# Optimization experiments

Measured on AMD Instinct MI355X. Metric: run time of the kernel, lower is better.

The kernel has to match this reference:

```python
import jax, jax.numpy as jnp
import numpy as np

DIM = 768
NUM_HEADS = 12
HEAD_DIM = DIM // NUM_HEADS
EPS = 1e-5


def setup_inputs() -> dict:
    key = jax.random.key(0)
    ks = jax.random.split(key, 9)
    s = 1.0 / np.sqrt(DIM)
    x = jax.random.normal(ks[0], (8, 1024, DIM), dtype=jnp.float32)
    Wq = jax.random.uniform(ks[1], (DIM, DIM), jnp.float32, -s, s)
    bq = jax.random.uniform(ks[2], (DIM,), jnp.float32, -s, s)
    Wk = jax.random.uniform(ks[3], (DIM, DIM), jnp.float32, -s, s)
    bk = jax.random.uniform(ks[4], (DIM,), jnp.float32, -s, s)
    Wv = jax.random.uniform(ks[5], (DIM, DIM), jnp.float32, -s, s)
    bv = jax.random.uniform(ks[6], (DIM,), jnp.float32, -s, s)
    Wo = jax.random.uniform(ks[7], (DIM, DIM), jnp.float32, -s, s)
    bo = jax.random.uniform(ks[8], (DIM,), jnp.float32, -s, s)
    ln_g = jnp.ones((DIM,), jnp.float32)
    ln_b = jnp.zeros((DIM,), jnp.float32)
    return {"x": x, "Wq": Wq, "bq": bq, "Wk": Wk, "bk": bk, "Wv": Wv,
            "bv": bv, "Wo": Wo, "bo": bo, "ln_g": ln_g, "ln_b": ln_b}


def _layernorm(h, g, b):
    mu = jnp.mean(h, axis=-1, keepdims=True)
    var = jnp.mean(jnp.square(h - mu), axis=-1, keepdims=True)
    return (h - mu) * jax.lax.rsqrt(var + EPS) * g + b


def reference(x, Wq, bq, Wk, bk, Wv, bv, Wo, bo, ln_g, ln_b):
    B, N, C = x.shape
    H, D = NUM_HEADS, HEAD_DIM
    scaling = D ** -0.5
    q = (x @ Wq.T + bq) * scaling          # [B,N,C]
    k = x @ Wk.T + bk
    v = x @ Wv.T + bv
    q = q.reshape(B, N, H, D).transpose(0, 2, 1, 3)  # [B,H,N,D]
    k = k.reshape(B, N, H, D).transpose(0, 2, 1, 3)
    v = v.reshape(B, N, H, D).transpose(0, 2, 1, 3)
    scores = jnp.einsum('bhnd,bhmd->bhnm', q, k)     # [B,H,N,N]
    probs = jax.nn.softmax(scores.astype(jnp.float32), axis=-1).astype(scores.dtype)
    attn = jnp.einsum('bhnm,bhmd->bhnd', probs, v)   # [B,H,N,D]
    attn = attn.transpose(0, 2, 1, 3).reshape(B, N, C)
    attn = _layernorm(attn, ln_g, ln_b)
    return attn @ Wo.T + bo
```

## Files before the change

### kernel.cpp

```cpp
#include <hip/hip_runtime.h>
#include <hip/hip_bf16.h>
#include <stdint.h>


using short8  = __attribute__((ext_vector_type(8))) short;
using short4v = __attribute__((ext_vector_type(4))) short;
using floatx4 = __attribute__((ext_vector_type(4))) float;

#define LOG2E 1.44269504088896340736f

typedef __attribute__((address_space(3))) uint32_t lds_u32;
typedef const __attribute__((address_space(1))) uint32_t glb_u32;
__device__ __forceinline__ void async_copy16(const void* g, void* l) {
  __builtin_amdgcn_global_load_lds((glb_u32*)g, (lds_u32*)l, 16, 0, 0);
}

__device__ __forceinline__ float b2f(int s) {
  return __builtin_bit_cast(float, (uint32_t)((uint16_t)s) << 16);
}
__device__ __forceinline__ short f2b(float f) {
  uint32_t u = __builtin_bit_cast(uint32_t, f);
  u += 0x7fffu + ((u >> 16) & 1u);
  return (short)(u >> 16);
}
__device__ __forceinline__ uint32_t pk2(float a, float b) {
#if defined(__has_builtin) && __has_builtin(__builtin_amdgcn_cvt_pk_bf16_f32)
  typedef __bf16 bf16x2 __attribute__((ext_vector_type(2)));
  return __builtin_bit_cast(uint32_t, __builtin_amdgcn_cvt_pk_bf16_f32(a, b));
#else
  return (uint32_t)(uint16_t)f2b(a) | ((uint32_t)(uint16_t)f2b(b) << 16);
#endif
}
__device__ __forceinline__ float loadf(const void* p, int idx, bool f32) {
  return f32 ? ((const float*)p)[idx] : b2f(((const short*)p)[idx]);
}
__device__ __forceinline__ short8 load8f(const void* p, int idx) {
  const float* q = (const float*)p + idx;
  float4 x0 = *(const float4*)q, x1 = *(const float4*)(q + 4);
  short8 v = {f2b(x0.x), f2b(x0.y), f2b(x0.z), f2b(x0.w),
              f2b(x1.x), f2b(x1.y), f2b(x1.z), f2b(x1.w)};
  return v;
}

__global__ __launch_bounds__(256) void cvt1_k(
    const void* __restrict__ x, const void* __restrict__ wq,
    const void* __restrict__ wk, const void* __restrict__ wv,
    const void* __restrict__ bq, const void* __restrict__ bk,
    const void* __restrict__ bv, short* __restrict__ xb,
    short* __restrict__ wqkvb, short* __restrict__ bqkvb,
    const unsigned short* __restrict__ probe) {
  if (probe[0] == 0x3F80u) return;
  int idx = blockIdx.x * 256 + threadIdx.x;
  if (idx < 786432) { *(short8*)&xb[idx * 8] = load8f(x, idx * 8); return; }
  idx -= 786432;
  if (idx < 73728) { *(short8*)&wqkvb[idx * 8] = load8f(wq, idx * 8); return; }
  idx -= 73728;
  if (idx < 73728) { *(short8*)&wqkvb[589824 + idx * 8] = load8f(wk, idx * 8); return; }
  idx -= 73728;
  if (idx < 73728) { *(short8*)&wqkvb[1179648 + idx * 8] = load8f(wv, idx * 8); return; }
  idx -= 73728;
  if (idx < 96) { *(short8*)&bqkvb[idx * 8] = load8f(bq, idx * 8); return; }
  idx -= 96;
  if (idx < 96) { *(short8*)&bqkvb[768 + idx * 8] = load8f(bk, idx * 8); return; }
  idx -= 96;
  if (idx < 96) { *(short8*)&bqkvb[1536 + idx * 8] = load8f(bv, idx * 8); return; }
}

__device__ __forceinline__ void gemm_core(const short* __restrict__ Ab,
                                          const short* __restrict__ Bb,
                                          short (*sA)[4096], short (*sB)[4096],
                                          floatx4 (&acc)[4][4]) {
  const int t = threadIdx.x;
  const int w = t >> 6, l = t & 63;
  const int lrow = l & 15, quad = l >> 4;
  const int rw = (w >> 1) * 64, cw = (w & 1) * 64;
  const int ci0 = t, ci1 = 256 + t;
  const int row0 = ci0 >> 2, ch0 = ci0 & 3;
  const int row1 = ci1 >> 2, ch1 = ci1 & 3;

  async_copy16(Ab + row0 * 768 + ch0 * 8, (char*)sA[0] + ci0 * 16);
  async_copy16(Bb + row0 * 768 + ch0 * 8, (char*)sB[0] + ci0 * 16);
  async_copy16(Ab + row1 * 768 + ch1 * 8, (char*)sA[0] + ci1 * 16);
  async_copy16(Bb + row1 * 768 + ch1 * 8, (char*)sB[0] + ci1 * 16);
  __syncthreads();

  for (int it = 0; it < 24; it++) {
    const int cur = it & 1;
    if (it < 23) {
      const int k0 = (it + 1) * 32, nxt = cur ^ 1;
      async_copy16(Ab + row0 * 768 + k0 + ch0 * 8, (char*)sA[nxt] + ci0 * 16);
      async_copy16(Bb + row0 * 768 + k0 + ch0 * 8, (char*)sB[nxt] + ci0 * 16);
      async_copy16(Ab + row1 * 768 + k0 + ch1 * 8, (char*)sA[nxt] + ci1 * 16);
      async_copy16(Bb + row1 * 768 + k0 + ch1 * 8, (char*)sB[nxt] + ci1 * 16);
    }
    short8 af[4], bf[4];
#pragma unroll
    for (int i = 0; i < 4; i++)
      af[i] = *(const short8*)&sA[cur][(rw + i * 16 + lrow) * 32 + quad * 8];
#pragma unroll
    for (int j = 0; j < 4; j++)
      bf[j] = *(const short8*)&sB[cur][(cw + j * 16 + lrow) * 32 + quad * 8];
#pragma unroll
    for (int i = 0; i < 4; i++)
#pragma unroll
      for (int j = 0; j < 4; j++)
        acc[i][j] =
            __builtin_amdgcn_mfma_f32_16x16x32_bf16(af[i], bf[j], acc[i][j], 0, 0, 0);
    __syncthreads();
  }
}

__global__ __launch_bounds__(256, 4) void gemm_qkv_k(
    const void* __restrict__ x, const short* __restrict__ xb,
    const void* __restrict__ Wq, const void* __restrict__ Wk,
    const void* __restrict__ Wv, const short* __restrict__ wqkvb,
    const void* __restrict__ bq, const void* __restrict__ bk,
    const void* __restrict__ bv, const short* __restrict__ bqkvb,
    short* __restrict__ qo, short* __restrict__ ko, short* __restrict__ vo,
    const unsigned short* __restrict__ probe) {
  __shared__ __align__(16) short sA[2][4096];
  __shared__ __align__(16) short sB[2][4096];
  const bool f32 = (probe[0] != 0x3F80u);
  const int atile = blockIdx.x, btile = blockIdx.y;
  const int sel = btile / 6;

  const short* Ab = (f32 ? xb : (const short*)x) + atile * 98304;
  const short* Bb;
  const short* biasb;
  if (f32) {
    Bb = wqkvb + btile * 98304;
    biasb = bqkvb + sel * 768;
  } else {
    const void* Wsel = sel == 0 ? Wq : (sel == 1 ? Wk : Wv);
    Bb = (const short*)Wsel + (btile - sel * 6) * 98304;
    biasb = (const short*)(sel == 0 ? bq : (sel == 1 ? bk : bv));
  }

  floatx4 acc[4][4] = {};
  gemm_core(Ab, Bb, sA, sB, acc);

  const int t = threadIdx.x, w = t >> 6, l = t & 63;
  const int lrow = l & 15, quad = l >> 4;
  const int rw = (w >> 1) * 64, cw = (w & 1) * 64;
  const int nbase = (btile - sel * 6) * 128;
#pragma unroll
  for (int i = 0; i < 4; i++) {
    const int ra0 = atile * 128 + rw + i * 16 + quad * 4;
    const int bidx = ra0 >> 10, n_in_b = ra0 & 1023;
#pragma unroll
    for (int j = 0; j < 4; j++) {
      const int cb = nbase + cw + j * 16 + lrow;
      const float bias = b2f(biasb[cb]);
      const int hh = cb >> 6, dd = cb & 63;
      if (sel == 2) {
        short4v pv;
#pragma unroll
        for (int r = 0; r < 4; r++) pv[r] = f2b(acc[i][j][r] + bias);
        const int n64 = n_in_b & 63;
        const int pos = ((n64 >> 2) & 3) * 8 + (n64 & 32) + ((n64 >> 4) & 1) * 4;
        *(short4v*)&vo[(bidx * 12 + hh) * 65536 + dd * 1024 + (n_in_b & ~63) + pos] = pv;
      } else {
        const int base = (bidx * 12 + hh) * 65536 + dd;
        short* dst = sel == 0 ? qo : ko;
#pragma unroll
        for (int r = 0; r < 4; r++) {
          float v = acc[i][j][r] + bias;
          if (sel == 0) v *= (0.125f * LOG2E);
          dst[base + (n_in_b + r) * 64] = f2b(v);
        }
      }
    }
  }
}

__global__ __launch_bounds__(256, 4) void gemm_out_k(
    const short* __restrict__ ln, const void* __restrict__ Wo,
    const short* __restrict__ wob, const void* __restrict__ bo,
    const short* __restrict__ bob, void* __restrict__ out,
    const unsigned short* __restrict__ probe) {
  __shared__ __align__(16) short sA[2][4096];
  __shared__ __align__(16) short sB[2][4096];
  const bool f32 = (probe[0] != 0x3F80u);
  const int atile = blockIdx.x, btile = blockIdx.y;
  const short* Ab = ln + atile * 98304;
  const short* Bb = (f32 ? wob : (const short*)Wo) + btile * 98304;
  const short* biasb = f32 ? bob : (const short*)bo;

  floatx4 acc[4][4] = {};
  gemm_core(Ab, Bb, sA, sB, acc);

  const int t = threadIdx.x, w = t >> 6, l = t & 63;
  const int lrow = l & 15, quad = l >> 4;
  const int rw = (w >> 1) * 64, cw = (w & 1) * 64;
#pragma unroll
  for (int i = 0; i < 4; i++) {
    const int ra0 = atile * 128 + rw + i * 16 + quad * 4;
#pragma unroll
    for (int j = 0; j < 4; j++) {
      const int cb = btile * 128 + cw + j * 16 + lrow;
      const float bias = b2f(biasb[cb]);
#pragma unroll
      for (int r = 0; r < 4; r++) {
        float v = acc[i][j][r] + bias;
        if (f32) ((float*)out)[(ra0 + r) * 768 + cb] = v;
        else     ((short*)out)[(ra0 + r) * 768 + cb] = f2b(v);
      }
    }
  }
}

__global__ __launch_bounds__(256, 5) void attn_k(const short* __restrict__ q,
                                                 const short* __restrict__ k,
                                                 const short* __restrict__ vt,
                                                 short* __restrict__ o) {
  __shared__ __align__(16) short sMem[2][8192];

  const int t = threadIdx.x, w = t >> 6, l = t & 63;
  const int lrow = l & 15, quad = l >> 4;
  const int bh = blockIdx.x, qt = blockIdx.y;
  const int b = bh / 12, h = bh % 12;
  const short* qb = q + bh * 65536 + qt * 4096;
  const short* kb = k + bh * 65536;
  const short* vb = vt + bh * 65536;

  const int srow = t >> 3, sgc = (t & 7) ^ (srow & 7);
  const short* kst = kb + srow * 64 + sgc * 8;
  const short* vst = vb + srow * 1024 + sgc * 8;

  const int swz0 = (quad ^ (lrow & 7)) * 16;
  const int swz1 = ((4 + quad) ^ (lrow & 7)) * 16;
  const char* s0 = (const char*)&sMem[0][0];
  const char* kp0 = s0 + lrow * 128 + swz0;
  const char* kp1 = s0 + lrow * 128 + swz1;
  const char* vp0 = s0 + 8192 + lrow * 128 + swz0;
  const char* vp1 = s0 + 8192 + lrow * 128 + swz1;

#pragma unroll
  for (int i = 0; i < 2; i++) {
    const int ci = i * 256 + t;
    const int row = ci >> 3, gc = (ci & 7) ^ (row & 7);
    async_copy16(qb + row * 64 + gc * 8, (char*)sMem[1] + ci * 16);
  }
  async_copy16(kst, (char*)sMem[0] + t * 16);
  async_copy16(kst + 2048, (char*)sMem[0] + 4096 + t * 16);
  async_copy16(vst, (char*)sMem[0] + 8192 + t * 16);
  async_copy16(vst + 32768, (char*)sMem[0] + 12288 + t * 16);
  __syncthreads();

  short8 qf[2];
  const int qr = w * 16 + lrow;
#pragma unroll
  for (int dc = 0; dc < 2; dc++)
    qf[dc] = *(const short8*)&sMem[1][qr * 64 + ((dc * 4 + quad) ^ (qr & 7)) * 8];
  __syncthreads();

  const short one_b = (short)0x3F80;
  const short8 ones8 = {one_b, one_b, one_b, one_b, one_b, one_b, one_b, one_b};
  floatx4 l_acc = {};
  floatx4 o_acc[4] = {};

#define ATTN_BODY(CUR, IT)                                                     \
  {                                                                            \
    if ((IT) < 15) {                                                           \
      const int nxt = (CUR) ^ 1;                                               \
      const short* ksrc = kst + ((IT) + 1) * 4096;                             \
      const short* vsrc = vst + ((IT) + 1) * 64;                               \
      async_copy16(ksrc, (char*)sMem[nxt] + t * 16);                           \
      async_copy16(ksrc + 2048, (char*)sMem[nxt] + 4096 + t * 16);             \
      async_copy16(vsrc, (char*)sMem[nxt] + 8192 + t * 16);                    \
      async_copy16(vsrc + 32768, (char*)sMem[nxt] + 12288 + t * 16);           \
    }                                                                          \
    short4v pf[4];                                                             \
    _Pragma("unroll")                                                          \
    for (int g = 0; g < 4; g++) {                                              \
      short8 kf0 = *(const short8*)(kp0 + (CUR) * 16384 + g * 2048);           \
      short8 kf1 = *(const short8*)(kp1 + (CUR) * 16384 + g * 2048);           \
      floatx4 st = {};                                                         \
      st = __builtin_amdgcn_mfma_f32_16x16x32_bf16(kf0, qf[0], st, 0, 0, 0);   \
      st = __builtin_amdgcn_mfma_f32_16x16x32_bf16(kf1, qf[1], st, 0, 0, 0);   \
      uint2 pp = {pk2(exp2f(st[0]), exp2f(st[1])),                             \
                  pk2(exp2f(st[2]), exp2f(st[3]))};                            \
      pf[g] = __builtin_bit_cast(short4v, pp);                                 \
    }                                                                          \
    const short8 pa0 =                                                         \
        __builtin_shufflevector(pf[0], pf[1], 0, 1, 2, 3, 4, 5, 6, 7);         \
    const short8 pa1 =                                                         \
        __builtin_shufflevector(pf[2], pf[3], 0, 1, 2, 3, 4, 5, 6, 7);         \
    l_acc = __builtin_amdgcn_mfma_f32_16x16x32_bf16(pa0, ones8, l_acc, 0, 0, 0); \
    l_acc = __builtin_amdgcn_mfma_f32_16x16x32_bf16(pa1, ones8, l_acc, 0, 0, 0); \
    _Pragma("unroll")                                                          \
    for (int j2 = 0; j2 < 4; j2++) {                                           \
      short8 vv0 = *(const short8*)(vp0 + (CUR) * 16384 + j2 * 2048);          \
      short8 vv1 = *(const short8*)(vp1 + (CUR) * 16384 + j2 * 2048);          \
      o_acc[j2] =                                                              \
          __builtin_amdgcn_mfma_f32_16x16x32_bf16(pa0, vv0, o_acc[j2], 0, 0, 0); \
      o_acc[j2] =                                                              \
          __builtin_amdgcn_mfma_f32_16x16x32_bf16(pa1, vv1, o_acc[j2], 0, 0, 0); \
    }                                                                          \
    __syncthreads();                                                           \
  }

  for (int it2 = 0; it2 < 8; it2++) {
    ATTN_BODY(0, it2 * 2)
    ATTN_BODY(1, it2 * 2 + 1)
  }
#undef ATTN_BODY

  float inv_l[4];
#pragma unroll
  for (int r = 0; r < 4; r++) inv_l[r] = 1.0f / l_acc[r];
  const int n0 = qt * 64 + w * 16 + quad * 4;
#pragma unroll
  for (int j2 = 0; j2 < 4; j2++) {
    const int d = j2 * 16 + lrow;
#pragma unroll
    for (int r = 0; r < 4; r++)
      o[(b * 1024 + n0 + r) * 768 + h * 64 + d] = f2b(o_acc[j2][r] * inv_l[r]);
  }
}

__global__ __launch_bounds__(256) void lncvt_k(const short* __restrict__ in,
                                               const void* __restrict__ g,
                                               const void* __restrict__ be,
                                               short* __restrict__ out,
                                               const void* __restrict__ wo,
                                               const void* __restrict__ bo,
                                               short* __restrict__ wob,
                                               short* __restrict__ bob,
                                               const unsigned short* __restrict__ probe) {
  const bool f32 = (probe[0] != 0x3F80u);
  if (blockIdx.x >= 2048) {
    if (!f32) return;
    int idx = (blockIdx.x - 2048) * 256 + threadIdx.x;
    if (idx < 73728) { *(short8*)&wob[idx * 8] = load8f(wo, idx * 8); return; }
    idx -= 73728;
    if (idx < 96) { *(short8*)&bob[idx * 8] = load8f(bo, idx * 8); }
    return;
  }
  const int w = threadIdx.x >> 6, l = threadIdx.x & 63;
  const int row = blockIdx.x * 4 + w;
  const short* rp = in + row * 768;
  float v[12];
  float s = 0.f, ss = 0.f;
#pragma unroll
  for (int c = 0; c < 3; c++) {
    ushort4 u = *(const ushort4*)&rp[(c * 64 + l) * 4];
    float f0 = b2f(u.x), f1 = b2f(u.y), f2 = b2f(u.z), f3 = b2f(u.w);
    v[c * 4 + 0] = f0; v[c * 4 + 1] = f1; v[c * 4 + 2] = f2; v[c * 4 + 3] = f3;
    s += (f0 + f1) + (f2 + f3);
    ss += (f0 * f0 + f1 * f1) + (f2 * f2 + f3 * f3);
  }
#pragma unroll
  for (int msk = 1; msk < 64; msk <<= 1) {
    s += __shfl_xor(s, msk);
    ss += __shfl_xor(ss, msk);
  }
  const float mu = s * (1.f / 768.f);
  const float rstd = rsqrtf(ss * (1.f / 768.f) - mu * mu + 1e-5f);
  short* op = out + row * 768;
#pragma unroll
  for (int c = 0; c < 3; c++) {
    const int base = (c * 64 + l) * 4;
    ushort4 r;
    r.x = (unsigned short)(unsigned)f2b((v[c * 4 + 0] - mu) * rstd * loadf(g, base + 0, f32) + loadf(be, base + 0, f32));
    r.y = (unsigned short)(unsigned)f2b((v[c * 4 + 1] - mu) * rstd * loadf(g, base + 1, f32) + loadf(be, base + 1, f32));
    r.z = (unsigned short)(unsigned)f2b((v[c * 4 + 2] - mu) * rstd * loadf(g, base + 2, f32) + loadf(be, base + 2, f32));
    r.w = (unsigned short)(unsigned)f2b((v[c * 4 + 3] - mu) * rstd * loadf(g, base + 3, f32) + loadf(be, base + 3, f32));
    *(ushort4*)&op[base] = r;
  }
}

extern "C" void kernel_launch(void* const* d_in, const int* in_sizes, int n_in,
                              void* d_out, int out_size, void* d_ws, size_t ws_size,
                              hipStream_t stream) {
  const void* x    = d_in[0];
  const void* Wq   = d_in[1];
  const void* bq   = d_in[2];
  const void* Wk   = d_in[3];
  const void* bk   = d_in[4];
  const void* Wv   = d_in[5];
  const void* bv   = d_in[6];
  const void* Wo   = d_in[7];
  const void* bo   = d_in[8];
  const void* ln_g = d_in[9];
  const void* ln_b = d_in[10];
  const unsigned short* probe = (const unsigned short*)d_in[9];

  char* ws = (char*)d_ws;
  const size_t SZ = 12582912;
  if (ws_size < 3 * SZ) return;
  short* qbuf = (short*)ws;
  short* kbuf = (short*)(ws + SZ);
  short* vtb  = (short*)(ws + 2 * SZ);

  char* outc = (char*)d_out;
  short* wqkvb = (short*)outc;
  short* bqkvb = (short*)(outc + 3538944);
  short* xb    = (short*)(outc + 12582912);
  short* wob   = (short*)(ws + SZ);
  short* bob   = (short*)(ws + SZ + 1179648);

  dim3 blk(256);
  cvt1_k<<<3938, blk, 0, stream>>>(x, Wq, Wk, Wv, bq, bk, bv, xb, wqkvb, bqkvb, probe);
  gemm_qkv_k<<<dim3(64, 18), blk, 0, stream>>>(x, xb, Wq, Wk, Wv, wqkvb, bq, bk, bv,
                                               bqkvb, qbuf, kbuf, vtb, probe);
  attn_k<<<dim3(96, 16), blk, 0, stream>>>(qbuf, kbuf, vtb, (short*)d_out);
  lncvt_k<<<2337, blk, 0, stream>>>((short*)d_out, ln_g, ln_b, qbuf,
                                    Wo, bo, wob, bob, probe);
  gemm_out_k<<<dim3(64, 6), blk, 0, stream>>>(qbuf, Wo, wob, bo, bob, d_out, probe);
}
```

Baseline: 230.7 us.

## Triple-buffer GEMM LDS staging with explicit vmcnt waits and one barrier

Moves the shared GEMM core from double to triple buffering in LDS, so loads are issued two k-steps ahead. Each iteration now waits on vmcnt, which keeps the next stage's copies in flight, and uses a single barrier instead of the old copy-then-sync pattern. The k-loop is fully unrolled. The extra LDS buffer means launch bounds drop from 4 to 3 blocks per CU, trading occupancy for deeper latency hiding.

```diff
diff --git a/kernel.cpp b/kernel.cpp
--- a/kernel.cpp
+++ b/kernel.cpp
@@ -77,22 +77,31 @@
   const int ci0 = t, ci1 = 256 + t;
   const int row0 = ci0 >> 2, ch0 = ci0 & 3;
   const int row1 = ci1 >> 2, ch1 = ci1 & 3;
-
-  async_copy16(Ab + row0 * 768 + ch0 * 8, (char*)sA[0] + ci0 * 16);
-  async_copy16(Bb + row0 * 768 + ch0 * 8, (char*)sB[0] + ci0 * 16);
-  async_copy16(Ab + row1 * 768 + ch1 * 8, (char*)sA[0] + ci1 * 16);
-  async_copy16(Bb + row1 * 768 + ch1 * 8, (char*)sB[0] + ci1 * 16);
-  __syncthreads();
-
+  const short* a0 = Ab + row0 * 768 + ch0 * 8;
+  const short* b0 = Bb + row0 * 768 + ch0 * 8;
+  const short* a1 = Ab + row1 * 768 + ch1 * 8;
+  const short* b1 = Bb + row1 * 768 + ch1 * 8;
+
+#define STAGE(BUF, K0)                                      \
+  async_copy16(a0 + (K0), (char*)sA[BUF] + ci0 * 16);       \
+  async_copy16(b0 + (K0), (char*)sB[BUF] + ci0 * 16);       \
+  async_copy16(a1 + (K0), (char*)sA[BUF] + ci1 * 16);       \
+  async_copy16(b1 + (K0), (char*)sB[BUF] + ci1 * 16);
+
+  STAGE(0, 0)
+  STAGE(1, 32)
+
+#pragma unroll
   for (int it = 0; it < 24; it++) {
-    const int cur = it & 1;
-    if (it < 23) {
-      const int k0 = (it + 1) * 32, nxt = cur ^ 1;
-      async_copy16(Ab + row0 * 768 + k0 + ch0 * 8, (char*)sA[nxt] + ci0 * 16);
-      async_copy16(Bb + row0 * 768 + k0 + ch0 * 8, (char*)sB[nxt] + ci0 * 16);
-      async_copy16(Ab + row1 * 768 + k0 + ch1 * 8, (char*)sA[nxt] + ci1 * 16);
-      async_copy16(Bb + row1 * 768 + k0 + ch1 * 8, (char*)sB[nxt] + ci1 * 16);
+    if (it < 23) { asm volatile("s_waitcnt vmcnt(4)" ::: "memory"); }
+    else         { asm volatile("s_waitcnt vmcnt(0)" ::: "memory"); }
+    __builtin_amdgcn_s_barrier();
+    asm volatile("" ::: "memory");
+    __builtin_amdgcn_sched_barrier(0);
+    if (it + 2 < 24) {
+      STAGE((it + 2) % 3, (it + 2) * 32)
     }
+    const int cur = it % 3;
     short8 af[4], bf[4];
 #pragma unroll
     for (int i = 0; i < 4; i++)
@@ -106,11 +115,11 @@
       for (int j = 0; j < 4; j++)
         acc[i][j] =
             __builtin_amdgcn_mfma_f32_16x16x32_bf16(af[i], bf[j], acc[i][j], 0, 0, 0);
-    __syncthreads();
-  }
-}
-
-__global__ __launch_bounds__(256, 4) void gemm_qkv_k(
+  }
+#undef STAGE
+}
+
+__global__ __launch_bounds__(256, 3) void gemm_qkv_k(
     const void* __restrict__ x, const short* __restrict__ xb,
     const void* __restrict__ Wq, const void* __restrict__ Wk,
     const void* __restrict__ Wv, const short* __restrict__ wqkvb,
@@ -118,8 +127,8 @@
     const void* __restrict__ bv, const short* __restrict__ bqkvb,
     short* __restrict__ qo, short* __restrict__ ko, short* __restrict__ vo,
     const unsigned short* __restrict__ probe) {
-  __shared__ __align__(16) short sA[2][4096];
-  __shared__ __align__(16) short sB[2][4096];
+  __shared__ __align__(16) short sA[3][4096];
+  __shared__ __align__(16) short sB[3][4096];
   const bool f32 = (probe[0] != 0x3F80u);
   const int atile = blockIdx.x, btile = blockIdx.y;
   const int sel = btile / 6;
@@ -173,13 +182,13 @@
   }
 }
 
-__global__ __launch_bounds__(256, 4) void gemm_out_k(
+__global__ __launch_bounds__(256, 3) void gemm_out_k(
     const short* __restrict__ ln, const void* __restrict__ Wo,
     const short* __restrict__ wob, const void* __restrict__ bo,
     const short* __restrict__ bob, void* __restrict__ out,
     const unsigned short* __restrict__ probe) {
-  __shared__ __align__(16) short sA[2][4096];
-  __shared__ __align__(16) short sB[2][4096];
+  __shared__ __align__(16) short sA[3][4096];
+  __shared__ __align__(16) short sB[3][4096];
   const bool f32 = (probe[0] != 0x3F80u);
   const int atile = blockIdx.x, btile = blockIdx.y;
   const short* Ab = ln + atile * 98304;
```

New measurement: 224.8 us. -2.6%, faster.
